# Optimization experiments

Measured on AMD Instinct MI355X. Metric: run time of the kernel, lower is better.

## Reference

```python
import jax, jax.numpy as jnp
import numpy as np

N_HEAD = 16
N_EMBED = 1024

def setup_inputs() -> dict:
    key = jax.random.key(0)
    ks = jax.random.split(key, 5)
    C = N_EMBED
    x = jax.random.normal(ks[0], (2, 2048, C), dtype=jnp.float32)
    # c_attn: Linear(C, 3C); c_proj: Linear(C, C). PyTorch Linear: y = x @ W.T + b
    w_attn = jax.random.normal(ks[1], (3 * C, C), dtype=jnp.float32) * (1.0 / np.sqrt(C))
    b_attn = jnp.zeros((3 * C,), dtype=jnp.float32)
    w_proj = jax.random.normal(ks[2], (C, C), dtype=jnp.float32) * (1.0 / np.sqrt(C))
    b_proj = jnp.zeros((C,), dtype=jnp.float32)
    return {"x": x, "w_attn": w_attn, "b_attn": b_attn, "w_proj": w_proj, "b_proj": b_proj}

def reference(x, w_attn, b_attn, w_proj, b_proj):
    B, T, C = x.shape
    H = N_HEAD
    D = C // H
    qkv = jnp.einsum('btc,fc->btf', x, w_attn) + b_attn  # [B,T,3C]
    q, k, v = jnp.split(qkv, 3, axis=-1)
    # [B,H,T,D]
    q = q.reshape(B, T, H, D).transpose(0, 2, 1, 3)
    k = k.reshape(B, T, H, D).transpose(0, 2, 1, 3)
    v = v.reshape(B, T, H, D).transpose(0, 2, 1, 3)
    att = jnp.einsum('bhqd,bhkd->bhqk', q, k) * (1.0 / np.sqrt(D))  # [B,H,T,T]
    causal = jnp.tril(jnp.ones((T, T), dtype=bool))
    att = jnp.where(causal[None, None], att, jnp.finfo(att.dtype).min)
    att = jax.nn.softmax(att, axis=-1)
    y = jnp.einsum('bhqk,bhkd->bhqd', att, v)  # [B,H,T,D]
    y = y.transpose(0, 2, 1, 3).reshape(B, T, C)
    return jnp.einsum('btc,fc->btf', y, w_proj) + b_proj
```

## Files before the change

### kernel.cpp

```cpp
#include <hip/hip_runtime.h>
#include <hip/hip_bf16.h>

typedef unsigned short u16;
typedef __attribute__((ext_vector_type(8))) short v8s;
typedef __attribute__((ext_vector_type(4))) short v4s;
typedef __attribute__((ext_vector_type(4))) float v4f;

__device__ __forceinline__ u16 f2bu(float f) {
  union { float f; unsigned u; } v; v.f = f;
  unsigned r = (v.u + 0x7fffu + ((v.u >> 16) & 1u)) >> 16;
  return (u16)r;
}
__device__ __forceinline__ v4s pack4(const v4f& a) {
  union { v4s s; __hip_bfloat162 h[2]; } u;
  u.h[0] = __float22bfloat162_rn(make_float2(a[0], a[1]));
  u.h[1] = __float22bfloat162_rn(make_float2(a[2], a[3]));
  return u.s;
}
__device__ __forceinline__ v8s pack8(const v4f& a, const v4f& b) {
  union { v8s s; __hip_bfloat162 h[4]; } u;
  u.h[0] = __float22bfloat162_rn(make_float2(a[0], a[1]));
  u.h[1] = __float22bfloat162_rn(make_float2(a[2], a[3]));
  u.h[2] = __float22bfloat162_rn(make_float2(b[0], b[1]));
  u.h[3] = __float22bfloat162_rn(make_float2(b[2], b[3]));
  return u.s;
}

__device__ __forceinline__ void g2l16(const u16* g, u16* l) {
  __builtin_amdgcn_global_load_lds((const __attribute__((address_space(1))) void*)g,
                                   (__attribute__((address_space(3))) void*)l,
                                   16, 0, 0);
}

__global__ __launch_bounds__(256) void cvt_bf16(const float* __restrict__ s0, u16* __restrict__ d0, int n0,
                                                const float* __restrict__ s1, u16* __restrict__ d1, int n1,
                                                const float* __restrict__ s2, u16* __restrict__ d2, int n2) {
  int total8 = (n0 + n1 + n2) >> 3;
  for (int i = blockIdx.x * blockDim.x + threadIdx.x; i < total8; i += gridDim.x * blockDim.x) {
    int e = i << 3;
    const float* s; u16* d;
    if (e < n0)            { s = s0 + e;            d = d0 + e; }
    else if (e < n0 + n1)  { s = s1 + (e - n0);     d = d1 + (e - n0); }
    else                   { s = s2 + (e - n0 - n1); d = d2 + (e - n0 - n1); }
    v4f a = *(const v4f*)s, b = *(const v4f*)(s + 4);
    *(v8s*)d = pack8(a, b);
  }
}

__global__ __launch_bounds__(256) void gemm_qkv(const u16* __restrict__ A,
                                                const u16* __restrict__ W,
                                                const float* __restrict__ bias,
                                                u16* __restrict__ o0,
                                                u16* __restrict__ o1,
                                                u16* __restrict__ o2) {
  constexpr int K = 1024;
  __shared__ __align__(16) u16 As[128 * 64];
  __shared__ __align__(16) u16 Bs[128 * 64];
  const int tid = threadIdx.x;
  const int w = tid >> 6, lane = tid & 63, l15 = lane & 15, quad = lane >> 4;
  const int wm = w & 1, wn = w >> 1;
  const int R0 = blockIdx.x * 128, C0 = blockIdx.y * 128;

  v4f acc[4][4] = {};
  const u16* Ag = A + (size_t)R0 * K;
  const u16* Wg = W + (size_t)C0 * K;

  int srow[4], scol[4], sdst[4];
#pragma unroll
  for (int i = 0; i < 4; ++i) {
    int p = (w * 4 + i) * 64 + lane;
    srow[i] = p >> 3;
    scol[i] = (p & 7) * 8;
    sdst[i] = (w * 4 + i) * 512;
  }

  for (int k0 = 0; k0 < K; k0 += 64) {
    if (k0) __syncthreads();
#pragma unroll
    for (int i = 0; i < 4; ++i) g2l16(Ag + srow[i] * K + k0 + scol[i], &As[sdst[i]]);
#pragma unroll
    for (int i = 0; i < 4; ++i) g2l16(Wg + srow[i] * K + k0 + scol[i], &Bs[sdst[i]]);
    __syncthreads();
#pragma unroll
    for (int kk = 0; kk < 2; ++kk) {
      v8s a[4], b[4];
#pragma unroll
      for (int m = 0; m < 4; ++m)
        a[m] = *(const v8s*)&As[(wm * 64 + m * 16 + l15) * 64 + (kk * 4 + quad) * 8];
#pragma unroll
      for (int n = 0; n < 4; ++n)
        b[n] = *(const v8s*)&Bs[(wn * 64 + n * 16 + l15) * 64 + (kk * 4 + quad) * 8];
#pragma unroll
      for (int m = 0; m < 4; ++m)
#pragma unroll
        for (int n = 0; n < 4; ++n)
          acc[m][n] = __builtin_amdgcn_mfma_f32_16x16x32_bf16(a[m], b[n], acc[m][n], 0, 0, 0);
    }
  }

#pragma unroll
  for (int n = 0; n < 4; ++n) {
    int f = C0 + wn * 64 + n * 16 + l15;
    float bv = bias[f];
#pragma unroll
    for (int m = 0; m < 4; ++m) {
      int r0 = R0 + wm * 64 + m * 16 + quad * 4;
      int which = f >> 10, c = f & 1023;
      int h = c >> 6, d = c & 63;
      int b = r0 >> 11, t = r0 & 2047;
      if (which == 2) {
        v4s pk;
#pragma unroll
        for (int reg = 0; reg < 4; ++reg) pk[reg] = (short)f2bu(acc[m][n][reg] + bv);
        *(v4s*)&o2[(((b << 4) + h) * 64 + d) * 2048 + t] = pk;
      } else {
        u16* dst = (which == 0) ? o0 : o1;
#pragma unroll
        for (int reg = 0; reg < 4; ++reg)
          dst[(((b << 4) + h) * 2048 + (t + reg)) * 64 + d] = f2bu(acc[m][n][reg] + bv);
      }
    }
  }
}

__global__ __launch_bounds__(256) void gemm_proj(const u16* __restrict__ A,
                                                 const u16* __restrict__ W,
                                                 const float* __restrict__ bias,
                                                 float* __restrict__ out) {
  constexpr int K = 1024;
  __shared__ __align__(16) u16 As[128 * 64];
  __shared__ __align__(16) u16 Bs[64 * 64];
  const int tid = threadIdx.x;
  const int w = tid >> 6, lane = tid & 63, l15 = lane & 15, quad = lane >> 4;
  const int wm = w & 1, wn = w >> 1;
  const int R0 = blockIdx.x * 128, C0 = blockIdx.y * 64;

  v4f acc[4][2] = {};
  const u16* Ag = A + (size_t)R0 * K;
  const u16* Wg = W + (size_t)C0 * K;

  int arow[4], acol[4], adst[4];
#pragma unroll
  for (int i = 0; i < 4; ++i) {
    int p = (w * 4 + i) * 64 + lane;
    arow[i] = p >> 3; acol[i] = (p & 7) * 8; adst[i] = (w * 4 + i) * 512;
  }
  int brow[2], bcol[2], bdst[2];
#pragma unroll
  for (int i = 0; i < 2; ++i) {
    int p = (w * 2 + i) * 64 + lane;
    brow[i] = p >> 3; bcol[i] = (p & 7) * 8; bdst[i] = (w * 2 + i) * 512;
  }

  for (int k0 = 0; k0 < K; k0 += 64) {
    if (k0) __syncthreads();
#pragma unroll
    for (int i = 0; i < 4; ++i) g2l16(Ag + arow[i] * K + k0 + acol[i], &As[adst[i]]);
#pragma unroll
    for (int i = 0; i < 2; ++i) g2l16(Wg + brow[i] * K + k0 + bcol[i], &Bs[bdst[i]]);
    __syncthreads();
#pragma unroll
    for (int kk = 0; kk < 2; ++kk) {
      v8s a[4], b[2];
#pragma unroll
      for (int m = 0; m < 4; ++m)
        a[m] = *(const v8s*)&As[(wm * 64 + m * 16 + l15) * 64 + (kk * 4 + quad) * 8];
#pragma unroll
      for (int n = 0; n < 2; ++n)
        b[n] = *(const v8s*)&Bs[(wn * 32 + n * 16 + l15) * 64 + (kk * 4 + quad) * 8];
#pragma unroll
      for (int m = 0; m < 4; ++m)
#pragma unroll
        for (int n = 0; n < 2; ++n)
          acc[m][n] = __builtin_amdgcn_mfma_f32_16x16x32_bf16(a[m], b[n], acc[m][n], 0, 0, 0);
    }
  }

#pragma unroll
  for (int n = 0; n < 2; ++n) {
    int f = C0 + wn * 32 + n * 16 + l15;
    float bv = bias[f];
#pragma unroll
    for (int m = 0; m < 4; ++m) {
      int r0 = R0 + wm * 64 + m * 16 + quad * 4;
#pragma unroll
      for (int reg = 0; reg < 4; ++reg)
        out[(size_t)(r0 + reg) * 1024 + f] = acc[m][n][reg] + bv;
    }
  }
}

#define SCL2 0.180336879f
__global__ __launch_bounds__(256, 2) void attn_kernel(const u16* __restrict__ Q,
                                                      const u16* __restrict__ Kt,
                                                      const u16* __restrict__ Vt,
                                                      u16* __restrict__ Y) {
  __shared__ __align__(16) u16 Ksh[2][64 * 64], Vsh[2][64 * 64];
  __shared__ __align__(16) u16 Psh[8 * 16 * 72];
  const int tid = threadIdx.x;
  const int w = tid >> 6, lane = tid & 63, l15 = lane & 15, quad = lane >> 4;
  const int pi = blockIdx.x, h = blockIdx.y, b = blockIdx.z;
  const int qtA = pi, qtB = 31 - pi;
  const int qA0 = qtA * 64, qB0 = qtB * 64;
  const int bh = b * 16 + h;
  const u16* qg = Q + bh * 131072;
  const u16* kg = Kt + bh * 131072;
  const u16* vg = Vt + bh * 131072;

  v8s aqA[2], aqB[2];
  {
    const u16* qrA = qg + (qA0 + w * 16 + l15) * 64;
    const u16* qrB = qg + (qB0 + w * 16 + l15) * 64;
#pragma unroll
    for (int kk = 0; kk < 2; ++kk) {
      aqA[kk] = *(const v8s*)(qrA + kk * 32 + quad * 8);
      aqB[kk] = *(const v8s*)(qrB + kk * 32 + quad * 8);
    }
  }

  v4f OA[4] = {}, OB[4] = {};
  float llA = 0.f, llB = 0.f;
  const int rowlim = w * 16 + l15;

  int srow[2], sgc[2], ssc[2];
  v8s tk[2], tv[2];
#pragma unroll
  for (int i = 0; i < 2; ++i) {
    int cc = (w * 2 + i) * 64 + lane;
    srow[i] = cc >> 3; int c = cc & 7;
    sgc[i] = c * 8; ssc[i] = ((c ^ (srow[i] & 7)) * 8);
    tk[i] = *(const v8s*)(kg + srow[i] * 64 + sgc[i]);
    tv[i] = *(const v8s*)(vg + srow[i] * 2048 + sgc[i]);
  }

  u16* PA = &Psh[(w * 2) * 16 * 72];
  u16* PB = &Psh[(w * 2 + 1) * 16 * 72];

  for (int kt = 0; kt <= qtB; ++kt) {
    const int k0 = kt * 64;
    const int buf = kt & 1;
#pragma unroll
    for (int i = 0; i < 2; ++i) {
      *(v8s*)&Ksh[buf][srow[i] * 64 + ssc[i]] = tk[i];
      *(v8s*)&Vsh[buf][srow[i] * 64 + ssc[i]] = tv[i];
    }
    __syncthreads();
    if (kt < qtB) {
      int kn = k0 + 64;
#pragma unroll
      for (int i = 0; i < 2; ++i) {
        tk[i] = *(const v8s*)(kg + (kn + srow[i]) * 64 + sgc[i]);
        tv[i] = *(const v8s*)(vg + srow[i] * 2048 + kn + sgc[i]);
      }
    }
    const bool doA = (kt <= qtA);
    const u16* Kb = Ksh[buf];
    const u16* Vb = Vsh[buf];

    v4f sA[4], sB[4];
#pragma unroll
    for (int nt = 0; nt < 4; ++nt) {
      v4f zb = {0.f, 0.f, 0.f, 0.f}, za = {0.f, 0.f, 0.f, 0.f};
#pragma unroll
      for (int kk = 0; kk < 2; ++kk) {
        v8s kf = *(const v8s*)&Kb[(nt * 16 + l15) * 64 + (((kk * 4 + quad) ^ (l15 & 7)) * 8)];
        zb = __builtin_amdgcn_mfma_f32_16x16x32_bf16(kf, aqB[kk], zb, 0, 0, 0);
        if (doA) za = __builtin_amdgcn_mfma_f32_16x16x32_bf16(kf, aqA[kk], za, 0, 0, 0);
      }
      sB[nt] = zb; sA[nt] = za;
    }

    {
      float rs = 0.f;
      if (kt == qtB) {
#pragma unroll
        for (int nt = 0; nt < 4; ++nt)
#pragma unroll
          for (int reg = 0; reg < 4; ++reg) {
            int kl = nt * 16 + quad * 4 + reg;
            float p = (kl <= rowlim) ? exp2f(sB[nt][reg] * SCL2) : 0.f;
            sB[nt][reg] = p; rs += p;
          }
      } else {
#pragma unroll
        for (int nt = 0; nt < 4; ++nt)
#pragma unroll
          for (int reg = 0; reg < 4; ++reg) {
            float p = exp2f(sB[nt][reg] * SCL2);
            sB[nt][reg] = p; rs += p;
          }
      }
      llB += rs;
#pragma unroll
      for (int nt = 0; nt < 4; ++nt)
        *(v4s*)&PB[l15 * 72 + nt * 16 + quad * 4] = pack4(sB[nt]);
    }
    if (doA) {
      float rs = 0.f;
      if (kt == qtA) {
#pragma unroll
        for (int nt = 0; nt < 4; ++nt)
#pragma unroll
          for (int reg = 0; reg < 4; ++reg) {
            int kl = nt * 16 + quad * 4 + reg;
            float p = (kl <= rowlim) ? exp2f(sA[nt][reg] * SCL2) : 0.f;
            sA[nt][reg] = p; rs += p;
          }
      } else {
#pragma unroll
        for (int nt = 0; nt < 4; ++nt)
#pragma unroll
          for (int reg = 0; reg < 4; ++reg) {
            float p = exp2f(sA[nt][reg] * SCL2);
            sA[nt][reg] = p; rs += p;
          }
      }
      llA += rs;
#pragma unroll
      for (int nt = 0; nt < 4; ++nt)
        *(v4s*)&PA[l15 * 72 + nt * 16 + quad * 4] = pack4(sA[nt]);
    }

    asm volatile("" ::: "memory");
    v8s apB[2], apA[2];
#pragma unroll
    for (int kk = 0; kk < 2; ++kk) {
      apB[kk] = *(const v8s*)&PB[l15 * 72 + kk * 32 + quad * 8];
      if (doA) apA[kk] = *(const v8s*)&PA[l15 * 72 + kk * 32 + quad * 8];
    }
#pragma unroll
    for (int nt = 0; nt < 4; ++nt)
#pragma unroll
      for (int kk = 0; kk < 2; ++kk) {
        v8s vf = *(const v8s*)&Vb[(nt * 16 + l15) * 64 + (((kk * 4 + quad) ^ (l15 & 7)) * 8)];
        OB[nt] = __builtin_amdgcn_mfma_f32_16x16x32_bf16(apB[kk], vf, OB[nt], 0, 0, 0);
        if (doA) OA[nt] = __builtin_amdgcn_mfma_f32_16x16x32_bf16(apA[kk], vf, OA[nt], 0, 0, 0);
      }
  }

  llB += __shfl_xor(llB, 16, 64); llB += __shfl_xor(llB, 32, 64);
  llA += __shfl_xor(llA, 16, 64); llA += __shfl_xor(llA, 32, 64);
  {
    float li = 1.f / llB, lO[4];
#pragma unroll
    for (int reg = 0; reg < 4; ++reg) lO[reg] = __shfl(li, quad * 4 + reg, 64);
    int tb2 = qB0 + w * 16 + quad * 4;
#pragma unroll
    for (int nt = 0; nt < 4; ++nt)
#pragma unroll
      for (int reg = 0; reg < 4; ++reg)
        Y[(b * 2048 + tb2 + reg) * 1024 + h * 64 + nt * 16 + l15] = f2bu(OB[nt][reg] * lO[reg]);
  }
  {
    float li = 1.f / llA, lO[4];
#pragma unroll
    for (int reg = 0; reg < 4; ++reg) lO[reg] = __shfl(li, quad * 4 + reg, 64);
    int tb2 = qA0 + w * 16 + quad * 4;
#pragma unroll
    for (int nt = 0; nt < 4; ++nt)
#pragma unroll
      for (int reg = 0; reg < 4; ++reg)
        Y[(b * 2048 + tb2 + reg) * 1024 + h * 64 + nt * 16 + l15] = f2bu(OA[nt][reg] * lO[reg]);
  }
}

extern "C" void kernel_launch(void* const* d_in, const int* in_sizes, int n_in,
                              void* d_out, int out_size, void* d_ws, size_t ws_size,
                              hipStream_t stream) {
  const float* x      = (const float*)d_in[0];
  const float* w_attn = (const float*)d_in[1];
  const float* b_attn = (const float*)d_in[2];
  const float* w_proj = (const float*)d_in[3];
  const float* b_proj = (const float*)d_in[4];
  float* out = (float*)d_out;
  char* ws = (char*)d_ws;
  u16* xb  = (u16*)(ws);
  u16* wab = (u16*)(ws + (size_t)( 8u << 20));
  u16* wpb = (u16*)(ws + (size_t)(14u << 20));
  u16* q   = (u16*)(ws + (size_t)(16u << 20));
  u16* k   = (u16*)(ws + (size_t)(24u << 20));
  u16* vt  = (u16*)(ws + (size_t)(32u << 20));
  u16* y   = (u16*)(ws + (size_t)(40u << 20));

  cvt_bf16<<<2048, 256, 0, stream>>>(x, xb, 4194304, w_attn, wab, 3145728, w_proj, wpb, 1048576);
  gemm_qkv<<<dim3(32, 24), 256, 0, stream>>>(xb, wab, b_attn, q, k, vt);
  attn_kernel<<<dim3(16, 16, 2), 256, 0, stream>>>(q, k, vt, y);
  gemm_proj<<<dim3(32, 16), 256, 0, stream>>>(y, wpb, b_proj, out);
}
```

Before: 186.5 us.

## Load K and V fragments directly from global into registers, dropping LDS staging

The attention kernel no longer stages K/V tiles through double-buffered shared memory with a block-wide barrier each step. Each wave now loads its MFMA K and V fragments straight from global memory into registers, and prefetches the next K tile after the QK MFMAs. This removes the LDS writes and reads and the __syncthreads per key tile. In exchange, each of the 4 waves loads the full K/V tile itself (4x redundant global/L2 traffic), register pressure rises, and the V loads are issued in the same iteration that uses them, so their latency is less hidden.

```diff
diff --git a/kernel.cpp b/kernel.cpp
--- a/kernel.cpp
+++ b/kernel.cpp
@@ -195,7 +195,6 @@
                                                       const u16* __restrict__ Kt,
                                                       const u16* __restrict__ Vt,
                                                       u16* __restrict__ Y) {
-  __shared__ __align__(16) u16 Ksh[2][64 * 64], Vsh[2][64 * 64];
   __shared__ __align__(16) u16 Psh[8 * 16 * 72];
   const int tid = threadIdx.x;
   const int w = tid >> 6, lane = tid & 63, l15 = lane & 15, quad = lane >> 4;
@@ -222,40 +221,29 @@
   float llA = 0.f, llB = 0.f;
   const int rowlim = w * 16 + l15;
 
-  int srow[2], sgc[2], ssc[2];
-  v8s tk[2], tv[2];
-#pragma unroll
-  for (int i = 0; i < 2; ++i) {
-    int cc = (w * 2 + i) * 64 + lane;
-    srow[i] = cc >> 3; int c = cc & 7;
-    sgc[i] = c * 8; ssc[i] = ((c ^ (srow[i] & 7)) * 8);
-    tk[i] = *(const v8s*)(kg + srow[i] * 64 + sgc[i]);
-    tv[i] = *(const v8s*)(vg + srow[i] * 2048 + sgc[i]);
-  }
+  const u16* kbase = kg + l15 * 64 + quad * 8;
+  const u16* vbase = vg + l15 * 2048 + quad * 8;
 
   u16* PA = &Psh[(w * 2) * 16 * 72];
   u16* PB = &Psh[(w * 2 + 1) * 16 * 72];
 
+  v8s kf[4][2];
+#pragma unroll
+  for (int nt = 0; nt < 4; ++nt)
+#pragma unroll
+    for (int kk = 0; kk < 2; ++kk)
+      kf[nt][kk] = *(const v8s*)(kbase + nt * 1024 + kk * 32);
+
   for (int kt = 0; kt <= qtB; ++kt) {
     const int k0 = kt * 64;
-    const int buf = kt & 1;
-#pragma unroll
-    for (int i = 0; i < 2; ++i) {
-      *(v8s*)&Ksh[buf][srow[i] * 64 + ssc[i]] = tk[i];
-      *(v8s*)&Vsh[buf][srow[i] * 64 + ssc[i]] = tv[i];
-    }
-    __syncthreads();
-    if (kt < qtB) {
-      int kn = k0 + 64;
-#pragma unroll
-      for (int i = 0; i < 2; ++i) {
-        tk[i] = *(const v8s*)(kg + (kn + srow[i]) * 64 + sgc[i]);
-        tv[i] = *(const v8s*)(vg + srow[i] * 2048 + kn + sgc[i]);
-      }
-    }
+    v8s vf[4][2];
+#pragma unroll
+    for (int nt = 0; nt < 4; ++nt)
+#pragma unroll
+      for (int kk = 0; kk < 2; ++kk)
+        vf[nt][kk] = *(const v8s*)(vbase + nt * 32768 + k0 + kk * 32);
+
     const bool doA = (kt <= qtA);
-    const u16* Kb = Ksh[buf];
-    const u16* Vb = Vsh[buf];
 
     v4f sA[4], sB[4];
 #pragma unroll
@@ -263,11 +251,18 @@
       v4f zb = {0.f, 0.f, 0.f, 0.f}, za = {0.f, 0.f, 0.f, 0.f};
 #pragma unroll
       for (int kk = 0; kk < 2; ++kk) {
-        v8s kf = *(const v8s*)&Kb[(nt * 16 + l15) * 64 + (((kk * 4 + quad) ^ (l15 & 7)) * 8)];
-        zb = __builtin_amdgcn_mfma_f32_16x16x32_bf16(kf, aqB[kk], zb, 0, 0, 0);
-        if (doA) za = __builtin_amdgcn_mfma_f32_16x16x32_bf16(kf, aqA[kk], za, 0, 0, 0);
+        zb = __builtin_amdgcn_mfma_f32_16x16x32_bf16(kf[nt][kk], aqB[kk], zb, 0, 0, 0);
+        if (doA) za = __builtin_amdgcn_mfma_f32_16x16x32_bf16(kf[nt][kk], aqA[kk], za, 0, 0, 0);
       }
       sB[nt] = zb; sA[nt] = za;
+    }
+
+    if (kt < qtB) {
+#pragma unroll
+      for (int nt = 0; nt < 4; ++nt)
+#pragma unroll
+        for (int kk = 0; kk < 2; ++kk)
+          kf[nt][kk] = *(const v8s*)(kbase + (k0 + 64) * 64 + nt * 1024 + kk * 32);
     }
 
     {
@@ -332,9 +327,8 @@
     for (int nt = 0; nt < 4; ++nt)
 #pragma unroll
       for (int kk = 0; kk < 2; ++kk) {
-        v8s vf = *(const v8s*)&Vb[(nt * 16 + l15) * 64 + (((kk * 4 + quad) ^ (l15 & 7)) * 8)];
-        OB[nt] = __builtin_amdgcn_mfma_f32_16x16x32_bf16(apB[kk], vf, OB[nt], 0, 0, 0);
-        if (doA) OA[nt] = __builtin_amdgcn_mfma_f32_16x16x32_bf16(apA[kk], vf, OA[nt], 0, 0, 0);
+        OB[nt] = __builtin_amdgcn_mfma_f32_16x16x32_bf16(apB[kk], vf[nt][kk], OB[nt], 0, 0, 0);
+        if (doA) OA[nt] = __builtin_amdgcn_mfma_f32_16x16x32_bf16(apA[kk], vf[nt][kk], OA[nt], 0, 0, 0);
       }
   }
 
```

New measurement: 255.4 us. 36.9% more time.
